# Kernel tuning notes

Measured on AMD Instinct MI355X. Metric: run time of the kernel, lower is better.

Reference implementation:

```python
import jax, jax.numpy as jnp
import numpy as np

B, T, M, C, H = 256, 512, 16, 16, 768  # batch, time, n_media, ctrl_dim, gru hidden


def setup_inputs() -> dict:
    key = jax.random.key(0)
    ks = jax.random.split(key, 16)
    def nrm(k, shape, s=0.05):
        return jax.random.normal(k, shape, jnp.float32) * s
    A = jnp.triu(jnp.ones((M, M), jnp.float32), 1)  # strict-upper DAG prior
    return dict(
        Xm=jax.random.uniform(ks[0], (B, T, M), jnp.float32),
        Xc=jax.random.normal(ks[1], (B, T, C), jnp.float32),
        R=jax.random.randint(ks[2], (B,), 0, 2),
        A=A,
        edge_w1=nrm(ks[3], (M, 2 * M)), edge_b1=jnp.zeros((M,), jnp.float32),
        edge_w2=nrm(ks[4], (M, M)), edge_b2=jnp.zeros((M,), jnp.float32),
        node_w=nrm(ks[5], (M, 2 * M)), node_b=jnp.zeros((M,), jnp.float32),
        W_ih=nrm(ks[6], (3 * H, M + C)), W_hh=nrm(ks[7], (3 * H, H)),
        b_ih=jnp.zeros((3 * H,), jnp.float32), b_hh=jnp.zeros((3 * H,), jnp.float32),
        wraw_w=nrm(ks[8], (M, H), 0.01), wraw_b=jnp.zeros((M,), jnp.float32),
        alpha=jnp.full((M,), 0.5, jnp.float32),
        hill_a=jax.random.uniform(ks[9], (M,), jnp.float32) * 0.8 + 0.6,
        hill_g=jax.random.uniform(ks[10], (M,), jnp.float32) * 0.3 + 0.1,
        ctrl_w=nrm(ks[11], (H, C)), ctrl_b=jnp.zeros((H,), jnp.float32),
        reg_emb=nrm(ks[12], (2, H)),
        bias=jnp.zeros((1,), jnp.float32),
        h0=jnp.zeros((1, 1, H), jnp.float32),
    )


def reference(Xm, Xc, R, A, edge_w1, edge_b1, edge_w2, edge_b2, node_w, node_b,
              W_ih, W_hh, b_ih, b_hh, wraw_w, wraw_b, alpha, hill_a, hill_g,
              ctrl_w, ctrl_b, reg_emb, bias, h0):
    Bq = Xm.shape[0]
    # --- CausalEncoder, fully batched over (B, T) ---
    send = Xm @ A.T                      # [B,T,M]
    recv = Xm @ A
    He = jax.nn.relu(jnp.concatenate([send, recv], -1) @ edge_w1.T + edge_b1)
    He = jax.nn.relu(He @ edge_w2.T + edge_b2)
    Z = jax.nn.relu(jnp.concatenate([Xm, He], -1) @ node_w.T + node_b)  # [B,T,M]
    # --- adstock: linear recurrence along time via scan ---
    a = jnp.clip(alpha, 0.0, 1.0)
    xt = jnp.swapaxes(Xm, 0, 1)          # [T,B,M]
    def ad_step(prev, x):
        cur = x + a * prev
        return cur, cur
    _, rest = jax.lax.scan(ad_step, xt[0], xt[1:])
    ads = jnp.swapaxes(jnp.concatenate([xt[:1], rest], 0), 0, 1)  # [B,T,M]
    cmax = jnp.maximum(jnp.max(ads, axis=1, keepdims=True), 1e-6)
    x_n = ads / cmax
    # --- hill saturation ---
    ha = jnp.clip(hill_a, 0.1, 3.0)
    hg = jnp.clip(hill_g, 0.1, 2.0)
    num = jnp.maximum(x_n, 0.0) ** ha
    hill = num / (num + hg ** ha + 1e-8)
    # --- GRU (PyTorch gate order r,z,n) via scan ---
    gru_in = jnp.concatenate([hill + Z, Xc], -1)       # [B,T,M+C]
    git = jnp.swapaxes(gru_in, 0, 1)                   # [T,B,M+C]
    h_init = jnp.broadcast_to(h0[0, 0], (Bq, h0.shape[-1]))
    def gru_step(h, x):
        gi = x @ W_ih.T + b_ih
        gh = h @ W_hh.T + b_hh
        ir, iz, inn = jnp.split(gi, 3, axis=-1)
        hr, hz, hn = jnp.split(gh, 3, axis=-1)
        r = jax.nn.sigmoid(ir + hr)
        z = jax.nn.sigmoid(iz + hz)
        n = jnp.tanh(inn + r * hn)
        h_new = (1.0 - z) * n + z * h
        return h_new, h_new
    _, hs = jax.lax.scan(gru_step, h_init, git)
    h_seq = jnp.swapaxes(hs, 0, 1)                     # [B,T,H]
    # --- coefficients + output heads ---
    w_pos = jax.nn.softplus(h_seq @ wraw_w.T + wraw_b)  # [B,T,M]
    w0 = 0.5 * jax.lax.stop_gradient(w_pos[:, 1]) + 0.5 * w_pos[:, 0]
    w_pos = w_pos.at[:, 0].set(w0)
    contrib = hill * w_pos
    media_term = contrib.sum(-1)                        # [B,T]
    ctrl_term = jax.nn.relu(Xc @ ctrl_w.T + ctrl_b).sum(-1) * 0.3
    reg_term = reg_emb[0].sum() * 0.3                   # original indexes with zeros
    y_scaled = media_term + ctrl_term + reg_term + bias[0]
    return y_scaled, w_pos, contrib
```

## Files before the change

### kernel.cpp

```cpp
#include <hip/hip_runtime.h>

typedef __bf16 bf16;
typedef bf16 bf16x8 __attribute__((ext_vector_type(8)));
typedef bf16 bf16x4 __attribute__((ext_vector_type(4)));
typedef float f32x4 __attribute__((ext_vector_type(4)));

#define MFMA16(a,b,c) __builtin_amdgcn_mfma_f32_16x16x32_bf16((a),(b),(c),0,0,0)

#define B_N 256
#define T_N 512
#define H_N 768
#define WROW 776
#define WIHROW 40

__device__ float    g_ctrl[B_N * T_N];
__device__ bf16     g_hbuf[2 * B_N * H_N];
__device__ unsigned g_flag[256 * 32];
__device__ unsigned g_members[8 * 32];
__device__ unsigned g_roster[8];
__device__ unsigned g_sync;

__device__ __forceinline__ float sigmoidf_(float x){ return 1.f/(1.f+__expf(-x)); }
__device__ __forceinline__ float tanhf_(float x){
  float e = __expf(-2.f*fabsf(x));
  float t = (1.f-e)/(1.f+e);
  return copysignf(t, x);
}
__device__ __forceinline__ float softplusf_(float x){
  return x > 20.f ? x : log1pf(__expf(x));
}

__global__ void k_zero() {
  const int tid = threadIdx.x;
  for (int i = tid; i < 256*32; i += 256) g_flag[i] = 0u;
  if (tid < 256) g_members[tid & 255] = 0u;
  if (tid < 8)   g_roster[tid] = 0u;
  if (tid == 0)  g_sync = 0u;
}

__global__ __launch_bounds__(256) void k_encode(
    const float* __restrict__ Xm, const float* __restrict__ Xc,
    const float* __restrict__ Aw,
    const float* __restrict__ ew1, const float* __restrict__ eb1,
    const float* __restrict__ ew2, const float* __restrict__ eb2,
    const float* __restrict__ nw,  const float* __restrict__ nb,
    const float* __restrict__ cw,  const float* __restrict__ cb,
    float* __restrict__ Zout)
{
  __shared__ float sA[16][16], sE1[16][32], sE2[16][16], sNW[16][32];
  __shared__ float sEB1[16], sEB2[16], sNB[16];
  __shared__ float sCW[768][16];
  __shared__ float sCB[768];
  const int tid = threadIdx.x;
  for (int i = tid; i < 256; i += 256) sA[i>>4][i&15] = Aw[i];
  for (int i = tid; i < 512; i += 256) sE1[i>>5][i&31] = ew1[i];
  for (int i = tid; i < 256; i += 256) sE2[i>>4][i&15] = ew2[i];
  for (int i = tid; i < 512; i += 256) sNW[i>>5][i&31] = nw[i];
  if (tid < 16) { sEB1[tid]=eb1[tid]; sEB2[tid]=eb2[tid]; sNB[tid]=nb[tid]; }
  for (int i = tid; i < 768*16; i += 256) sCW[i>>4][i&15] = cw[i];
  for (int i = tid; i < 768; i += 256) sCB[i] = cb[i];
  __syncthreads();
  const int idx = blockIdx.x*256 + tid;
  const float* xmp = Xm + (size_t)idx*16;
  const float* xcp = Xc + (size_t)idx*16;
  float xm[16], xc[16];
  #pragma unroll
  for (int j=0;j<4;j++){
    *(f32x4*)&xm[j*4] = *(const f32x4*)(xmp + j*4);
    *(f32x4*)&xc[j*4] = *(const f32x4*)(xcp + j*4);
  }
  float snd[16], rcv[16];
  #pragma unroll
  for (int i=0;i<16;i++){
    float s=0.f, r=0.f;
    #pragma unroll
    for (int j=0;j<16;j++){ s += xm[j]*sA[i][j]; r += xm[j]*sA[j][i]; }
    snd[i]=s; rcv[i]=r;
  }
  float he[16];
  #pragma unroll
  for (int i=0;i<16;i++){
    float a = sEB1[i];
    #pragma unroll
    for (int k=0;k<16;k++) a += snd[k]*sE1[i][k];
    #pragma unroll
    for (int k=0;k<16;k++) a += rcv[k]*sE1[i][16+k];
    he[i] = fmaxf(a, 0.f);
  }
  float he2[16];
  #pragma unroll
  for (int i=0;i<16;i++){
    float a = sEB2[i];
    #pragma unroll
    for (int k=0;k<16;k++) a += he[k]*sE2[i][k];
    he2[i] = fmaxf(a, 0.f);
  }
  float* zp = Zout + (size_t)idx*16;
  #pragma unroll
  for (int m=0;m<16;m++){
    float a = sNB[m];
    #pragma unroll
    for (int k=0;k<16;k++) a += xm[k]*sNW[m][k];
    #pragma unroll
    for (int k=0;k<16;k++) a += he2[k]*sNW[m][16+k];
    zp[m] = fmaxf(a, 0.f);
  }
  float cs = 0.f;
  for (int i=0;i<768;i++){
    float a = sCB[i];
    #pragma unroll
    for (int k=0;k<16;k++) a += xc[k]*sCW[i][k];
    cs += fmaxf(a, 0.f);
  }
  g_ctrl[idx] = cs * 0.3f;
}

__global__ __launch_bounds__(64) void k_adstock(
    const float* __restrict__ Xm, const float* __restrict__ alpha,
    const float* __restrict__ hill_a, const float* __restrict__ hill_g,
    float* __restrict__ Zio, float* __restrict__ hill_out)
{
  const int gid = blockIdx.x*64 + threadIdx.x;
  const int b = gid >> 4, m = gid & 15;
  float a  = fminf(fmaxf(alpha[m],  0.f),  1.f);
  float ha = fminf(fmaxf(hill_a[m], 0.1f), 3.f);
  float hg = fminf(fmaxf(hill_g[m], 0.1f), 2.f);
  float gpow = __powf(hg, ha);
  const float* xp = Xm + (size_t)b*T_N*16 + m;
  float prev = 0.f, cmax = 0.f;
  for (int t=0;t<T_N;t++){ float x = xp[(size_t)t*16]; prev = x + a*prev; cmax = fmaxf(cmax, prev); }
  cmax = fmaxf(cmax, 1e-6f);
  float inv = 1.f/cmax;
  prev = 0.f;
  float* zp  = Zio      + (size_t)b*T_N*16 + m;
  float* hp  = hill_out + (size_t)b*T_N*16 + m;
  for (int t=0;t<T_N;t++){
    float x = xp[(size_t)t*16];
    prev = x + a*prev;
    float xn  = fmaxf(prev*inv, 0.f);
    float num = __powf(xn, ha);
    float h   = num / (num + gpow + 1e-8f);
    float z   = zp[(size_t)t*16];
    hp[(size_t)t*16] = h;
    zp[(size_t)t*16] = h + z;
  }
}

__device__ __forceinline__ void poll_flags(unsigned midx, unsigned val) {
  int tries = 0;
  for (;;) {
    unsigned v = __hip_atomic_load(&g_flag[midx], __ATOMIC_RELAXED, __HIP_MEMORY_SCOPE_AGENT);
    if (__ballot(v >= val) == ~0ull) break;
    if (++tries > (1<<18)) break;
    if (tries > 8) __builtin_amdgcn_s_sleep(1);
  }
  __builtin_amdgcn_fence(__ATOMIC_ACQUIRE, "workgroup");
}

__global__ __launch_bounds__(256, 1) void k_gru(
    const float* __restrict__ Xc,
    const float* __restrict__ Wih, const float* __restrict__ Whh,
    const float* __restrict__ bih, const float* __restrict__ bhh,
    const float* __restrict__ wraww, const float* __restrict__ wrawb,
    const float* __restrict__ regemb, const float* __restrict__ bias,
    const float* __restrict__ h0,
    float* __restrict__ hillZ,
    float* __restrict__ hill,
    float* __restrict__ outy)
{
  __shared__ __align__(16) bf16 sW[88*WROW];
  __shared__ __align__(16) bf16 sWih[72*WIHROW];
  __shared__ float sGH[32][84];
  __shared__ float sGIN[32][36];
  __shared__ float sHm[32][24];
  __shared__ float sHD[32][17];
  __shared__ float sBih[72], sBhh[72];
  __shared__ float sWrb[16];
  __shared__ float sScal[2];
  __shared__ unsigned sGP[2];

  const int tid = threadIdx.x;
  const int wave = tid >> 6, lane = tid & 63;
  const int quad = lane >> 4, l16 = lane & 15;

  if (tid == 0) {
    unsigned x;
    asm volatile("s_getreg_b32 %0, hwreg(HW_REG_XCC_ID, 0, 32)" : "=s"(x));
    x &= 7u;
    unsigned slot = __hip_atomic_fetch_add(&g_roster[x], 1u,
                        __ATOMIC_RELAXED, __HIP_MEMORY_SCOPE_AGENT);
    if (slot < 32u)
      __hip_atomic_store(&g_members[x*32u + slot], (unsigned)blockIdx.x,
                         __ATOMIC_RELAXED, __HIP_MEMORY_SCOPE_AGENT);
    sGP[0] = x; sGP[1] = slot & 31u;
    __hip_atomic_fetch_add(&g_sync, 1u, __ATOMIC_RELEASE, __HIP_MEMORY_SCOPE_AGENT);
    int tries = 0;
    while (__hip_atomic_load(&g_sync, __ATOMIC_ACQUIRE, __HIP_MEMORY_SCOPE_AGENT) < 256u) {
      if (++tries > (1<<20)) break;
      __builtin_amdgcn_s_sleep(1);
    }
  }
  __syncthreads();
  const int g = (int)sGP[0], p = (int)sGP[1];
  const int j0 = p*24;
  const unsigned midx = __hip_atomic_load(&g_members[g*32 + (lane & 31)],
                            __ATOMIC_RELAXED, __HIP_MEMORY_SCOPE_AGENT) * 32u;
  const unsigned myflag = (unsigned)blockIdx.x * 32u;

  for (int c = tid; c < 88*192; c += 256) {
    int rl = c / 192, off = (c - rl*192)*4;
    const float* src = (rl < 72)
        ? &Whh[(size_t)((rl/24)*768 + j0 + (rl%24))*768 + off]
        : &wraww[(size_t)(rl-72)*768 + off];
    f32x4 w = *(const f32x4*)src;
    bf16x4 v; v[0]=(bf16)w[0]; v[1]=(bf16)w[1]; v[2]=(bf16)w[2]; v[3]=(bf16)w[3];
    *(bf16x4*)&sW[rl*WROW + off] = v;
  }
  for (int c = tid; c < 72*8; c += 256) {
    int rl = c >> 3, off = (c & 7)*4;
    int grow = (rl/24)*768 + j0 + (rl%24);
    f32x4 w = *(const f32x4*)&Wih[(size_t)grow*32 + off];
    bf16x4 v; v[0]=(bf16)w[0]; v[1]=(bf16)w[1]; v[2]=(bf16)w[2]; v[3]=(bf16)w[3];
    *(bf16x4*)&sWih[rl*WIHROW + off] = v;
  }
  if (tid < 72) {
    int grow = (tid/24)*768 + j0 + (tid%24);
    sBih[tid] = bih[grow];
    sBhh[tid] = bhh[grow];
  }
  if (tid >= 128 && tid < 144) sWrb[tid-128] = wrawb[tid-128];
  if (wave == 0) {
    float s = 0.f;
    for (int k = lane; k < 768; k += 64) s += regemb[k];
    #pragma unroll
    for (int off = 32; off; off >>= 1) s += __shfl_xor(s, off, 64);
    if (lane == 0) { sScal[0] = 0.3f*s; sScal[1] = bias[0]; }
  }
  {
    unsigned* hb = (unsigned*)g_hbuf;
    for (int e = tid; e < 384; e += 256) {
      int b = e/12, j = (e - b*12)*2;
      float f0 = h0[j0+j], f1 = h0[j0+j+1];
      sHm[b][j] = f0; sHm[b][j+1] = f1;
      union { bf16 h[2]; unsigned u; } pk;
      pk.h[0] = (bf16)f0; pk.h[1] = (bf16)f1;
      hb[((size_t)(g*32+b)*H_N + j0 + j) >> 1] = pk.u;
    }
  }
  __syncthreads();
  if (tid == 0)
    __hip_atomic_store(&g_flag[myflag], 1u, __ATOMIC_RELAXED, __HIP_MEMORY_SCOPE_AGENT);

  const int mi = wave >> 1;
  const bool lowN = !(wave & 1);
  const int batch_l = l16 + mi*16;
  const int gb = g*32 + batch_l;
  const int bq = g*32 + p;
  const float regt = sScal[0], bias0 = sScal[1];
  const int r0 = lowN ? l16        : 48 + l16;
  const int r1 = lowN ? 16 + l16   : min(64 + l16, 71);
  const int rX = lowN ? 32 + l16   : 72 + l16;
  const int rh = 72 + l16;

  bf16x8 bw0[24], bw1[24];
  #pragma unroll
  for (int kt = 0; kt < 24; kt++) {
    const int ko = kt*32 + quad*8;
    bw0[kt] = *(const bf16x8*)&sW[r0*WROW + ko];
    bw1[kt] = *(const bf16x8*)&sW[r1*WROW + ko];
  }
  const bf16x8 wf0 = *(const bf16x8*)&sWih[r0*WIHROW + quad*8];
  const bf16x8 wf1 = *(const bf16x8*)&sWih[r1*WIHROW + quad*8];
  const bf16x8 wf2 = lowN ? *(const bf16x8*)&sWih[(32+l16)*WIHROW + quad*8] : wf0;

  float wp0_r = 0.f, hl0_r = 0.f, ct0_r = 0.f;

  f32x4 xf0, xf1;
  {
    const float* hz = hillZ + (size_t)gb*T_N*16;
    const float* xr = Xc    + (size_t)gb*T_N*16;
    const float* src = (quad < 2) ? (hz + quad*8) : (xr + (quad-2)*8);
    xf0 = *(const f32x4*)src;
    xf1 = *(const f32x4*)(src + 4);
  }
  float hl_pf = 0.f, ct_pf = 0.f;
  if (tid < 16) {
    hl_pf = hill[(size_t)bq*T_N*16 + tid];
    if (tid == 0) ct_pf = g_ctrl[(size_t)bq*T_N];
  }

  const bf16* hb_base = g_hbuf;
  int par = 0;
  for (int t = 0; t < T_N; t++) {
    f32x4 a0 = {0.f,0.f,0.f,0.f}, a1 = a0, a2 = a0, gi0 = a0, gi1 = a0, hd = a0;
    {
      bf16x8 ax;
      ax[0]=(bf16)xf0[0]; ax[1]=(bf16)xf0[1]; ax[2]=(bf16)xf0[2]; ax[3]=(bf16)xf0[3];
      ax[4]=(bf16)xf1[0]; ax[5]=(bf16)xf1[1]; ax[6]=(bf16)xf1[2]; ax[7]=(bf16)xf1[3];
      if (lowN) {
        a0 = MFMA16(ax, wf0, a0);
        a1 = MFMA16(ax, wf1, a1);
        a2 = MFMA16(ax, wf2, a2);
      } else {
        gi0 = MFMA16(ax, wf0, gi0);
        gi1 = MFMA16(ax, wf1, gi1);
      }
    }
    poll_flags(midx, (unsigned)(t + 1));
    bf16x8 hf[24];
    {
      const bf16* hrow = hb_base + (size_t)par*B_N*H_N + (size_t)gb*H_N + quad*8;
      #pragma unroll
      for (int kt = 0; kt < 24; kt++) {
        asm volatile("global_load_dwordx4 %0, %1, off sc0"
                     : "=v"(hf[kt]) : "v"(hrow + kt*32) : "memory");
      }
      asm volatile("s_waitcnt vmcnt(0)"
          : "+v"(hf[0]),"+v"(hf[1]),"+v"(hf[2]),"+v"(hf[3]),
            "+v"(hf[4]),"+v"(hf[5]),"+v"(hf[6]),"+v"(hf[7]) :: "memory");
      asm volatile(""
          : "+v"(hf[8]),"+v"(hf[9]),"+v"(hf[10]),"+v"(hf[11]),
            "+v"(hf[12]),"+v"(hf[13]),"+v"(hf[14]),"+v"(hf[15]));
      asm volatile(""
          : "+v"(hf[16]),"+v"(hf[17]),"+v"(hf[18]),"+v"(hf[19]),
            "+v"(hf[20]),"+v"(hf[21]),"+v"(hf[22]),"+v"(hf[23]));
    }
    {
      const int tn = (t + 1 < T_N) ? t + 1 : T_N - 1;
      const float* hz = hillZ + ((size_t)gb*T_N + tn)*16;
      const float* xr = Xc    + ((size_t)gb*T_N + tn)*16;
      const float* src = (quad < 2) ? (hz + quad*8) : (xr + (quad-2)*8);
      xf0 = *(const f32x4*)src;
      xf1 = *(const f32x4*)(src + 4);
    }
    #pragma unroll
    for (int kt = 0; kt < 24; kt++) {
      const int ko = kt*32 + quad*8;
      a0 = MFMA16(hf[kt], bw0[kt], a0);
      a1 = MFMA16(hf[kt], bw1[kt], a1);
      if (lowN) a2 = MFMA16(hf[kt], *(const bf16x8*)&sW[rX*WROW + ko], a2);
      else      hd = MFMA16(hf[kt], *(const bf16x8*)&sW[rX*WROW + ko], hd);
    }
    {
      const int rb = mi*16 + quad*4;
      const int c0 = lowN ? l16 : 48 + l16;
      const int c1 = lowN ? 16 + l16 : 64 + l16;
      #pragma unroll
      for (int r = 0; r < 4; r++) {
        sGH[rb + r][c0] = a0[r];
        sGH[rb + r][c1] = a1[r];
        if (lowN) sGH[rb + r][32 + l16] = a2[r];
        else { sGIN[rb + r][l16] = gi0[r]; sGIN[rb + r][16 + l16] = gi1[r];
               sHD[rb + r][l16] = hd[r]; }
      }
    }
    __syncthreads();
    float hd_s = 0.f;
    if (tid < 16) hd_s = sHD[p][tid];
    if (tid >= 32) {
      unsigned* hnxt = (unsigned*)(g_hbuf + (size_t)(1-par)*B_N*H_N);
      for (int e = tid - 32; e < 384; e += 224) {
        int b = e/12, j = (e - b*12)*2;
        float hn0, hn1;
        {
          float rr = sigmoidf_(sGH[b][j]    + sBih[j]    + sBhh[j]);
          float zz = sigmoidf_(sGH[b][24+j] + sBih[24+j] + sBhh[24+j]);
          float hh = sGH[b][48+j] + sBhh[48+j];
          float in_ = sGIN[b][j]  + sBih[48+j];
          float nn = tanhf_(in_ + rr*hh);
          hn0 = (1.f-zz)*nn + zz*sHm[b][j];
        }
        {
          int j1 = j+1;
          float rr = sigmoidf_(sGH[b][j1]    + sBih[j1]    + sBhh[j1]);
          float zz = sigmoidf_(sGH[b][24+j1] + sBih[24+j1] + sBhh[24+j1]);
          float hh = sGH[b][48+j1] + sBhh[48+j1];
          float in_ = sGIN[b][j1]  + sBih[48+j1];
          float nn = tanhf_(in_ + rr*hh);
          hn1 = (1.f-zz)*nn + zz*sHm[b][j1];
        }
        sHm[b][j] = hn0; sHm[b][j+1] = hn1;
        union { bf16 h[2]; unsigned u; } pk;
        pk.h[0] = (bf16)hn0; pk.h[1] = (bf16)hn1;
        hnxt[((size_t)(g*32+b)*H_N + j0 + j) >> 1] = pk.u;
      }
    }
    __syncthreads();
    if (tid == 0)
      __hip_atomic_store(&g_flag[myflag], (unsigned)(t + 2), __ATOMIC_RELAXED, __HIP_MEMORY_SCOPE_AGENT);
    if (t > 0 && tid < 16) {
      const int tt = t - 1;
      float wp = softplusf_(hd_s + sWrb[tid]);
      float hl = hl_pf;
      if (tt == 0) { wp0_r = wp; hl0_r = hl; ct0_r = ct_pf; }
      else {
        size_t o = (size_t)bq*T_N + tt;
        float cv = hl*wp;
        hillZ[o*16 + tid] = wp;
        hill[o*16 + tid]  = cv;
        float cs = cv;
        cs += __shfl_xor(cs, 8, 64);
        cs += __shfl_xor(cs, 4, 64);
        cs += __shfl_xor(cs, 2, 64);
        cs += __shfl_xor(cs, 1, 64);
        if (tid == 0) outy[o] = cs + ct_pf + regt + bias0;
        if (tt == 1) {
          float w0 = 0.5f*(wp + wp0_r);
          float c0v = hl0_r*w0;
          size_t o0 = (size_t)bq*T_N;
          hillZ[o0*16 + tid] = w0;
          hill[o0*16 + tid]  = c0v;
          float cs0 = c0v;
          cs0 += __shfl_xor(cs0, 8, 64);
          cs0 += __shfl_xor(cs0, 4, 64);
          cs0 += __shfl_xor(cs0, 2, 64);
          cs0 += __shfl_xor(cs0, 1, 64);
          if (tid == 0) outy[o0] = cs0 + ct0_r + regt + bias0;
        }
      }
    }
    if (tid < 16) {
      hl_pf = hill[((size_t)bq*T_N + t)*16 + tid];
      if (tid == 0) ct_pf = g_ctrl[(size_t)bq*T_N + t];
    }
    par ^= 1;
  }
  if (wave & 1) {
    poll_flags(midx, (unsigned)(T_N + 1));
    const bf16* hrow = hb_base + (size_t)par*B_N*H_N + (size_t)gb*H_N + quad*8;
    f32x4 hd = {0.f,0.f,0.f,0.f};
    bf16x8 hf[24];
    #pragma unroll
    for (int kt = 0; kt < 24; kt++) {
      asm volatile("global_load_dwordx4 %0, %1, off sc0"
                   : "=v"(hf[kt]) : "v"(hrow + kt*32) : "memory");
    }
    asm volatile("s_waitcnt vmcnt(0)"
        : "+v"(hf[0]),"+v"(hf[1]),"+v"(hf[2]),"+v"(hf[3]),
          "+v"(hf[4]),"+v"(hf[5]),"+v"(hf[6]),"+v"(hf[7]) :: "memory");
    asm volatile(""
        : "+v"(hf[8]),"+v"(hf[9]),"+v"(hf[10]),"+v"(hf[11]),
          "+v"(hf[12]),"+v"(hf[13]),"+v"(hf[14]),"+v"(hf[15]));
    asm volatile(""
        : "+v"(hf[16]),"+v"(hf[17]),"+v"(hf[18]),"+v"(hf[19]),
          "+v"(hf[20]),"+v"(hf[21]),"+v"(hf[22]),"+v"(hf[23]));
    #pragma unroll
    for (int kt = 0; kt < 24; kt++) {
      const int ko = kt*32 + quad*8;
      hd = MFMA16(hf[kt], *(const bf16x8*)&sW[rh*WROW + ko], hd);
    }
    const int rb = mi*16 + quad*4;
    #pragma unroll
    for (int r = 0; r < 4; r++) sHD[rb + r][l16] = hd[r];
  }
  __syncthreads();
  if (tid < 16) {
    const int tt = T_N - 1;
    float wp = softplusf_(sHD[p][tid] + sWrb[tid]);
    float hl = hill[((size_t)bq*T_N + tt)*16 + tid];
    size_t o = (size_t)bq*T_N + tt;
    float cv = hl*wp;
    hillZ[o*16 + tid] = wp;
    hill[o*16 + tid]  = cv;
    float cs = cv;
    cs += __shfl_xor(cs, 8, 64);
    cs += __shfl_xor(cs, 4, 64);
    cs += __shfl_xor(cs, 2, 64);
    cs += __shfl_xor(cs, 1, 64);
    if (tid == 0) outy[o] = cs + g_ctrl[o] + regt + bias0;
  }
}

extern "C" void kernel_launch(void* const* d_in, const int* in_sizes, int n_in,
                              void* d_out, int out_size, void* d_ws, size_t ws_size,
                              hipStream_t stream) {
  const float* Xm    = (const float*)d_in[0];
  const float* Xc    = (const float*)d_in[1];
  const float* Aw    = (const float*)d_in[3];
  const float* ew1   = (const float*)d_in[4];
  const float* eb1   = (const float*)d_in[5];
  const float* ew2   = (const float*)d_in[6];
  const float* eb2   = (const float*)d_in[7];
  const float* nw    = (const float*)d_in[8];
  const float* nb    = (const float*)d_in[9];
  const float* Wih   = (const float*)d_in[10];
  const float* Whh   = (const float*)d_in[11];
  const float* bih   = (const float*)d_in[12];
  const float* bhh   = (const float*)d_in[13];
  const float* wraww = (const float*)d_in[14];
  const float* wrawb = (const float*)d_in[15];
  const float* alpha = (const float*)d_in[16];
  const float* hilla = (const float*)d_in[17];
  const float* hillg = (const float*)d_in[18];
  const float* cw    = (const float*)d_in[19];
  const float* cb    = (const float*)d_in[20];
  const float* regemb= (const float*)d_in[21];
  const float* bias  = (const float*)d_in[22];
  const float* h0    = (const float*)d_in[23];

  float* outy = (float*)d_out;
  float* outw = outy + 256*512;
  float* outc = outw + 256*512*16;

  k_zero<<<1, 256, 0, stream>>>();
  k_encode<<<512, 256, 0, stream>>>(Xm, Xc, Aw, ew1, eb1, ew2, eb2, nw, nb, cw, cb,
                                    outw);
  k_adstock<<<64, 64, 0, stream>>>(Xm, alpha, hilla, hillg, outw, outc);
  k_gru<<<dim3(256), dim3(256), 0, stream>>>(
      Xc, Wih, Whh, bih, bhh, wraww, wrawb, regemb, bias, h0,
      outw, outc, outy);
}
```

Before: 3.584 ms.

## Split GRU batch into two half-groups and pipeline MFMA with gate update wave

Restructures the persistent GRU kernel so each block handles its 32 batch rows as two 16-row halves. Three waves run the recurrent MFMAs for one half while a fourth wave applies the gate nonlinearities and publishes h for the other half, with separate per-half flags. Weight fragments move into registers loaded straight from global memory, and the h loads are split into staged waitcnts that interleave with even/odd accumulators. This aims to hide cross-block sync and gate-math latency behind matrix work. The cost is a more intricate flag protocol with timeout-based polling and extra barriers per half-step.

```diff
diff --git a/kernel.cpp b/kernel.cpp
--- a/kernel.cpp
+++ b/kernel.cpp
@@ -4,6 +4,7 @@
 typedef bf16 bf16x8 __attribute__((ext_vector_type(8)));
 typedef bf16 bf16x4 __attribute__((ext_vector_type(4)));
 typedef float f32x4 __attribute__((ext_vector_type(4)));
+typedef float f32x2 __attribute__((ext_vector_type(2)));
 
 #define MFMA16(a,b,c) __builtin_amdgcn_mfma_f32_16x16x32_bf16((a),(b),(c),0,0,0)
 
@@ -11,11 +12,10 @@
 #define T_N 512
 #define H_N 768
 #define WROW 776
-#define WIHROW 40
 
 __device__ float    g_ctrl[B_N * T_N];
 __device__ bf16     g_hbuf[2 * B_N * H_N];
-__device__ unsigned g_flag[256 * 32];
+__device__ unsigned g_flag[256 * 64];
 __device__ unsigned g_members[8 * 32];
 __device__ unsigned g_roster[8];
 __device__ unsigned g_sync;
@@ -29,11 +29,19 @@
 __device__ __forceinline__ float softplusf_(float x){
   return x > 20.f ? x : log1pf(__expf(x));
 }
+__device__ __forceinline__ bf16x8 ld_bf8(const float* p){
+  f32x4 a = *(const f32x4*)p;
+  f32x4 b = *(const f32x4*)(p + 4);
+  bf16x8 v;
+  v[0]=(bf16)a[0]; v[1]=(bf16)a[1]; v[2]=(bf16)a[2]; v[3]=(bf16)a[3];
+  v[4]=(bf16)b[0]; v[5]=(bf16)b[1]; v[6]=(bf16)b[2]; v[7]=(bf16)b[3];
+  return v;
+}
 
 __global__ void k_zero() {
   const int tid = threadIdx.x;
-  for (int i = tid; i < 256*32; i += 256) g_flag[i] = 0u;
-  if (tid < 256) g_members[tid & 255] = 0u;
+  for (int i = tid; i < 256*64; i += 256) g_flag[i] = 0u;
+  if (tid < 256) g_members[tid] = 0u;
   if (tid < 8)   g_roster[tid] = 0u;
   if (tid == 0)  g_sync = 0u;
 }
@@ -146,16 +154,20 @@
   }
 }
 
-__device__ __forceinline__ void poll_flags(unsigned midx, unsigned val) {
-  int tries = 0;
+__device__ __forceinline__ bool poll_flags(unsigned midx, unsigned val) {
+  int tries = 0; bool ok = true;
   for (;;) {
     unsigned v = __hip_atomic_load(&g_flag[midx], __ATOMIC_RELAXED, __HIP_MEMORY_SCOPE_AGENT);
     if (__ballot(v >= val) == ~0ull) break;
-    if (++tries > (1<<18)) break;
+    if (++tries > (1<<18)) { ok = false; break; }
     if (tries > 8) __builtin_amdgcn_s_sleep(1);
   }
   __builtin_amdgcn_fence(__ATOMIC_ACQUIRE, "workgroup");
-}
+  return ok;
+}
+
+#define HL(i, OFF) asm volatile("global_load_dwordx4 %0, %1, off offset:" OFF " sc0" \
+      : "=v"(hf[i]) : "v"(hsrc) : "memory")
 
 __global__ __launch_bounds__(256, 1) void k_gru(
     const float* __restrict__ Xc,
@@ -168,16 +180,15 @@
     float* __restrict__ hill,
     float* __restrict__ outy)
 {
-  __shared__ __align__(16) bf16 sW[88*WROW];
-  __shared__ __align__(16) bf16 sWih[72*WIHROW];
-  __shared__ float sGH[32][84];
-  __shared__ float sGIN[32][36];
-  __shared__ float sHm[32][24];
-  __shared__ float sHD[32][17];
-  __shared__ float sBih[72], sBhh[72];
+  __shared__ __align__(16) bf16 sW2[48*WROW];
+  __shared__ __align__(16) float sGH2[2][16][100];
+  __shared__ __align__(16) float sGIN[2][16][32];
+  __shared__ __align__(16) float sHm[32][28];
+  __shared__ __align__(16) float sBih[72], sBhh[72];
   __shared__ float sWrb[16];
   __shared__ float sScal[2];
   __shared__ unsigned sGP[2];
+  __shared__ unsigned sTok[2];
 
   const int tid = threadIdx.x;
   const int wave = tid >> 6, lane = tid & 63;
@@ -193,6 +204,7 @@
       __hip_atomic_store(&g_members[x*32u + slot], (unsigned)blockIdx.x,
                          __ATOMIC_RELAXED, __HIP_MEMORY_SCOPE_AGENT);
     sGP[0] = x; sGP[1] = slot & 31u;
+    sTok[0] = 0u; sTok[1] = 0u;
     __hip_atomic_fetch_add(&g_sync, 1u, __ATOMIC_RELEASE, __HIP_MEMORY_SCOPE_AGENT);
     int tries = 0;
     while (__hip_atomic_load(&g_sync, __ATOMIC_ACQUIRE, __HIP_MEMORY_SCOPE_AGENT) < 256u) {
@@ -203,25 +215,23 @@
   __syncthreads();
   const int g = (int)sGP[0], p = (int)sGP[1];
   const int j0 = p*24;
-  const unsigned midx = __hip_atomic_load(&g_members[g*32 + (lane & 31)],
-                            __ATOMIC_RELAXED, __HIP_MEMORY_SCOPE_AGENT) * 32u;
-  const unsigned myflag = (unsigned)blockIdx.x * 32u;
-
-  for (int c = tid; c < 88*192; c += 256) {
+  const int s_own = (p >= 16) ? 1 : 0;
+  const int bqL = p & 15;
+  const int bq = g*32 + p;
+  const unsigned member = __hip_atomic_load(&g_members[g*32 + (lane & 31)],
+                              __ATOMIC_RELAXED, __HIP_MEMORY_SCOPE_AGENT);
+  const unsigned midx0 = member * 64u;
+  const unsigned myflag = (unsigned)blockIdx.x * 64u;
+
+  for (int c = tid; c < 48*192; c += 256) {
     int rl = c / 192, off = (c - rl*192)*4;
-    const float* src = (rl < 72)
-        ? &Whh[(size_t)((rl/24)*768 + j0 + (rl%24))*768 + off]
-        : &wraww[(size_t)(rl-72)*768 + off];
-    f32x4 w = *(const f32x4*)src;
+    int L = (rl < 16) ? (16 + rl) : ((rl < 32) ? (32 + rl) : (48 + rl));
+    f32x4 w;
+    if (L < 72)      w = *(const f32x4*)&Whh[(size_t)((L/24)*768 + j0 + (L%24))*768 + off];
+    else if (L < 88) w = *(const f32x4*)&wraww[(size_t)(L-72)*768 + off];
+    else             { w[0]=0.f; w[1]=0.f; w[2]=0.f; w[3]=0.f; }
     bf16x4 v; v[0]=(bf16)w[0]; v[1]=(bf16)w[1]; v[2]=(bf16)w[2]; v[3]=(bf16)w[3];
-    *(bf16x4*)&sW[rl*WROW + off] = v;
-  }
-  for (int c = tid; c < 72*8; c += 256) {
-    int rl = c >> 3, off = (c & 7)*4;
-    int grow = (rl/24)*768 + j0 + (rl%24);
-    f32x4 w = *(const f32x4*)&Wih[(size_t)grow*32 + off];
-    bf16x4 v; v[0]=(bf16)w[0]; v[1]=(bf16)w[1]; v[2]=(bf16)w[2]; v[3]=(bf16)w[3];
-    *(bf16x4*)&sWih[rl*WIHROW + off] = v;
+    *(bf16x4*)&sW2[rl*WROW + off] = v;
   }
   if (tid < 72) {
     int grow = (tid/24)*768 + j0 + (tid%24);
@@ -230,12 +240,39 @@
   }
   if (tid >= 128 && tid < 144) sWrb[tid-128] = wrawb[tid-128];
   if (wave == 0) {
-    float s = 0.f;
-    for (int k = lane; k < 768; k += 64) s += regemb[k];
-    #pragma unroll
-    for (int off = 32; off; off >>= 1) s += __shfl_xor(s, off, 64);
-    if (lane == 0) { sScal[0] = 0.3f*s; sScal[1] = bias[0]; }
-  }
+    float sacc = 0.f;
+    for (int k = lane; k < 768; k += 64) sacc += regemb[k];
+    #pragma unroll
+    for (int off = 32; off; off >>= 1) sacc += __shfl_xor(sacc, off, 64);
+    if (lane == 0) { sScal[0] = 0.3f*sacc; sScal[1] = bias[0]; }
+  }
+
+  bf16x8 bw[24];
+  bf16x8 wf0, wf1, wfg;
+  #pragma unroll
+  for (int i = 0; i < 8; i++) { wf0[i]=(bf16)0.f; wf1[i]=(bf16)0.f; wfg[i]=(bf16)0.f; }
+  if (wave < 3) {
+    const int L = wave*32 + l16;
+    const float* rowA = (L < 72)
+        ? Whh + (size_t)((L/24)*768 + j0 + (L%24))*768
+        : wraww + (size_t)(L-72)*768;
+    #pragma unroll
+    for (int kk = 0; kk < 24; kk++) bw[kk] = ld_bf8(rowA + kk*32 + quad*8);
+    if (wave == 0) {
+      const int La = l16, Lb = 16 + l16;
+      wf0 = ld_bf8(Wih + (size_t)((La/24)*768 + j0 + (La%24))*32 + quad*8);
+      wf1 = ld_bf8(Wih + (size_t)((Lb/24)*768 + j0 + (Lb%24))*32 + quad*8);
+    } else if (wave == 1) {
+      const int La = 32 + l16, Lb = 48 + l16;
+      wf0 = ld_bf8(Wih + (size_t)((La/24)*768 + j0 + (La%24))*32 + quad*8);
+      wfg = ld_bf8(Wih + (size_t)((Lb/24)*768 + j0 + (Lb%24))*32 + quad*8);
+    } else {
+      const int Lb = 64 + l16;
+      if (Lb < 72)
+        wfg = ld_bf8(Wih + (size_t)((Lb/24)*768 + j0 + (Lb%24))*32 + quad*8);
+    }
+  }
+
   {
     unsigned* hb = (unsigned*)g_hbuf;
     for (int e = tid; e < 384; e += 256) {
@@ -248,215 +285,244 @@
     }
   }
   __syncthreads();
-  if (tid == 0)
-    __hip_atomic_store(&g_flag[myflag], 1u, __ATOMIC_RELAXED, __HIP_MEMORY_SCOPE_AGENT);
-
-  const int mi = wave >> 1;
-  const bool lowN = !(wave & 1);
-  const int batch_l = l16 + mi*16;
-  const int gb = g*32 + batch_l;
-  const int bq = g*32 + p;
+  if (tid == 0) {
+    __hip_atomic_store(&g_flag[myflag],      1u, __ATOMIC_RELAXED, __HIP_MEMORY_SCOPE_AGENT);
+    __hip_atomic_store(&g_flag[myflag + 32], 1u, __ATOMIC_RELAXED, __HIP_MEMORY_SCOPE_AGENT);
+  }
   const float regt = sScal[0], bias0 = sScal[1];
-  const int r0 = lowN ? l16        : 48 + l16;
-  const int r1 = lowN ? 16 + l16   : min(64 + l16, 71);
-  const int rX = lowN ? 32 + l16   : 72 + l16;
-  const int rh = 72 + l16;
-
-  bf16x8 bw0[24], bw1[24];
-  #pragma unroll
-  for (int kt = 0; kt < 24; kt++) {
-    const int ko = kt*32 + quad*8;
-    bw0[kt] = *(const bf16x8*)&sW[r0*WROW + ko];
-    bw1[kt] = *(const bf16x8*)&sW[r1*WROW + ko];
-  }
-  const bf16x8 wf0 = *(const bf16x8*)&sWih[r0*WIHROW + quad*8];
-  const bf16x8 wf1 = *(const bf16x8*)&sWih[r1*WIHROW + quad*8];
-  const bf16x8 wf2 = lowN ? *(const bf16x8*)&sWih[(32+l16)*WIHROW + quad*8] : wf0;
 
   float wp0_r = 0.f, hl0_r = 0.f, ct0_r = 0.f;
+  float hl_pf = 0.f, ct_pf = 0.f;
+  if (wave == 3 && lane < 16) {
+    hl_pf = hill[(size_t)bq*T_N*16 + lane];
+    if (lane == 0) ct_pf = g_ctrl[(size_t)bq*T_N];
+  }
 
   f32x4 xf0, xf1;
-  {
-    const float* hz = hillZ + (size_t)gb*T_N*16;
-    const float* xr = Xc    + (size_t)gb*T_N*16;
-    const float* src = (quad < 2) ? (hz + quad*8) : (xr + (quad-2)*8);
-    xf0 = *(const f32x4*)src;
-    xf1 = *(const f32x4*)(src + 4);
-  }
-  float hl_pf = 0.f, ct_pf = 0.f;
-  if (tid < 16) {
-    hl_pf = hill[(size_t)bq*T_N*16 + tid];
-    if (tid == 0) ct_pf = g_ctrl[(size_t)bq*T_N];
-  }
-
-  const bf16* hb_base = g_hbuf;
-  int par = 0;
-  for (int t = 0; t < T_N; t++) {
-    f32x4 a0 = {0.f,0.f,0.f,0.f}, a1 = a0, a2 = a0, gi0 = a0, gi1 = a0, hd = a0;
-    {
-      bf16x8 ax;
-      ax[0]=(bf16)xf0[0]; ax[1]=(bf16)xf0[1]; ax[2]=(bf16)xf0[2]; ax[3]=(bf16)xf0[3];
-      ax[4]=(bf16)xf1[0]; ax[5]=(bf16)xf1[1]; ax[6]=(bf16)xf1[2]; ax[7]=(bf16)xf1[3];
-      if (lowN) {
-        a0 = MFMA16(ax, wf0, a0);
-        a1 = MFMA16(ax, wf1, a1);
-        a2 = MFMA16(ax, wf2, a2);
-      } else {
-        gi0 = MFMA16(ax, wf0, gi0);
-        gi1 = MFMA16(ax, wf1, gi1);
-      }
-    }
-    poll_flags(midx, (unsigned)(t + 1));
-    bf16x8 hf[24];
-    {
-      const bf16* hrow = hb_base + (size_t)par*B_N*H_N + (size_t)gb*H_N + quad*8;
-      #pragma unroll
-      for (int kt = 0; kt < 24; kt++) {
-        asm volatile("global_load_dwordx4 %0, %1, off sc0"
-                     : "=v"(hf[kt]) : "v"(hrow + kt*32) : "memory");
-      }
-      asm volatile("s_waitcnt vmcnt(0)"
+  xf0[0]=0.f; xf0[1]=0.f; xf0[2]=0.f; xf0[3]=0.f; xf1 = xf0;
+  if (wave < 3) {
+    const int gb0 = g*32 + l16;
+    const float* srcx = (quad < 2)
+        ? hillZ + (size_t)gb0*T_N*16 + quad*8
+        : Xc    + (size_t)gb0*T_N*16 + (quad-2)*8;
+    xf0 = *(const f32x4*)srcx;
+    xf1 = *(const f32x4*)(srcx + 4);
+  }
+  const bf16* wlds = &sW2[(size_t)(wave*16 + l16)*WROW + quad*8];
+
+  #pragma unroll 1
+  for (int k = 0; k <= 2*T_N; k++) {
+    const int t = k >> 1, s = k & 1;
+    if (wave < 3) {
+      if (k < 2*T_N) {
+        {
+          unsigned tok = sTok[s];
+          if (tok < (unsigned)(t + 1))
+            poll_flags(midx0 + (unsigned)(s*32), (unsigned)(t + 1));
+          else
+            __builtin_amdgcn_fence(__ATOMIC_ACQUIRE, "workgroup");
+        }
+        const bf16* hsrc = g_hbuf + (size_t)(t&1)*B_N*H_N
+                         + (size_t)(g*32 + s*16 + l16)*H_N + quad*8;
+        f32x4 xn0, xn1;
+        {
+          const int sn = s ^ 1;
+          int tn = s ? (t + 1) : t; if (tn >= T_N) tn = T_N - 1;
+          const int gbn = g*32 + sn*16 + l16;
+          const float* srcx = (quad < 2)
+              ? hillZ + ((size_t)gbn*T_N + tn)*16 + quad*8
+              : Xc    + ((size_t)gbn*T_N + tn)*16 + (quad-2)*8;
+          asm volatile("global_load_dwordx4 %0, %2, off\n\t"
+                       "global_load_dwordx4 %1, %2, off offset:16"
+                       : "=v"(xn0), "=v"(xn1) : "v"(srcx) : "memory");
+        }
+        bf16x8 hf[24];
+        HL(0,"0");    HL(1,"64");   HL(2,"128");  HL(3,"192");
+        HL(4,"256");  HL(5,"320");  HL(6,"384");  HL(7,"448");
+        HL(8,"512");  HL(9,"576");  HL(10,"640"); HL(11,"704");
+        HL(12,"768"); HL(13,"832"); HL(14,"896"); HL(15,"960");
+        HL(16,"1024");HL(17,"1088");HL(18,"1152");HL(19,"1216");
+        HL(20,"1280");HL(21,"1344");HL(22,"1408");HL(23,"1472");
+        bf16x8 ax;
+        ax[0]=(bf16)xf0[0]; ax[1]=(bf16)xf0[1]; ax[2]=(bf16)xf0[2]; ax[3]=(bf16)xf0[3];
+        ax[4]=(bf16)xf1[0]; ax[5]=(bf16)xf1[1]; ax[6]=(bf16)xf1[2]; ax[7]=(bf16)xf1[3];
+        f32x4 az; az[0]=0.f; az[1]=0.f; az[2]=0.f; az[3]=0.f;
+        f32x4 a0e=az, a0o=az, a1e=az, a1o=az, gi=az;
+        if (wave == 0)      { a0e = MFMA16(ax, wf0, a0e); a1e = MFMA16(ax, wf1, a1e); }
+        else if (wave == 1) { a0e = MFMA16(ax, wf0, a0e); gi  = MFMA16(ax, wfg, gi);  }
+        else                { gi  = MFMA16(ax, wfg, gi); }
+        asm volatile("s_waitcnt vmcnt(16)"
           : "+v"(hf[0]),"+v"(hf[1]),"+v"(hf[2]),"+v"(hf[3]),
             "+v"(hf[4]),"+v"(hf[5]),"+v"(hf[6]),"+v"(hf[7]) :: "memory");
-      asm volatile(""
+        #pragma unroll
+        for (int kk = 0; kk < 8; kk += 2) {
+          a0e = MFMA16(hf[kk],   bw[kk],   a0e);
+          a1e = MFMA16(hf[kk],   *(const bf16x8*)&wlds[kk*32],     a1e);
+          a0o = MFMA16(hf[kk+1], bw[kk+1], a0o);
+          a1o = MFMA16(hf[kk+1], *(const bf16x8*)&wlds[(kk+1)*32], a1o);
+        }
+        asm volatile("s_waitcnt vmcnt(8)"
           : "+v"(hf[8]),"+v"(hf[9]),"+v"(hf[10]),"+v"(hf[11]),
-            "+v"(hf[12]),"+v"(hf[13]),"+v"(hf[14]),"+v"(hf[15]));
-      asm volatile(""
+            "+v"(hf[12]),"+v"(hf[13]),"+v"(hf[14]),"+v"(hf[15]) :: "memory");
+        #pragma unroll
+        for (int kk = 8; kk < 16; kk += 2) {
+          a0e = MFMA16(hf[kk],   bw[kk],   a0e);
+          a1e = MFMA16(hf[kk],   *(const bf16x8*)&wlds[kk*32],     a1e);
+          a0o = MFMA16(hf[kk+1], bw[kk+1], a0o);
+          a1o = MFMA16(hf[kk+1], *(const bf16x8*)&wlds[(kk+1)*32], a1o);
+        }
+        asm volatile("s_waitcnt vmcnt(0)"
           : "+v"(hf[16]),"+v"(hf[17]),"+v"(hf[18]),"+v"(hf[19]),
-            "+v"(hf[20]),"+v"(hf[21]),"+v"(hf[22]),"+v"(hf[23]));
-    }
-    {
-      const int tn = (t + 1 < T_N) ? t + 1 : T_N - 1;
-      const float* hz = hillZ + ((size_t)gb*T_N + tn)*16;
-      const float* xr = Xc    + ((size_t)gb*T_N + tn)*16;
-      const float* src = (quad < 2) ? (hz + quad*8) : (xr + (quad-2)*8);
-      xf0 = *(const f32x4*)src;
-      xf1 = *(const f32x4*)(src + 4);
-    }
-    #pragma unroll
-    for (int kt = 0; kt < 24; kt++) {
-      const int ko = kt*32 + quad*8;
-      a0 = MFMA16(hf[kt], bw0[kt], a0);
-      a1 = MFMA16(hf[kt], bw1[kt], a1);
-      if (lowN) a2 = MFMA16(hf[kt], *(const bf16x8*)&sW[rX*WROW + ko], a2);
-      else      hd = MFMA16(hf[kt], *(const bf16x8*)&sW[rX*WROW + ko], hd);
-    }
-    {
-      const int rb = mi*16 + quad*4;
-      const int c0 = lowN ? l16 : 48 + l16;
-      const int c1 = lowN ? 16 + l16 : 64 + l16;
+            "+v"(hf[20]),"+v"(hf[21]),"+v"(hf[22]),"+v"(hf[23]),
+            "+v"(xn0),"+v"(xn1) :: "memory");
+        #pragma unroll
+        for (int kk = 16; kk < 24; kk += 2) {
+          a0e = MFMA16(hf[kk],   bw[kk],   a0e);
+          a1e = MFMA16(hf[kk],   *(const bf16x8*)&wlds[kk*32],     a1e);
+          a0o = MFMA16(hf[kk+1], bw[kk+1], a0o);
+          a1o = MFMA16(hf[kk+1], *(const bf16x8*)&wlds[(kk+1)*32], a1o);
+        }
+        xf0 = xn0; xf1 = xn1;
+        f32x4 A0 = a0e + a0o, A1 = a1e + a1o;
+        {
+          const int c0 = wave*32 + l16;
+          #pragma unroll
+          for (int r = 0; r < 4; r++) {
+            const int rb = quad*4 + r;
+            sGH2[s][rb][c0]    = A0[r];
+            sGH2[s][rb][c0+16] = A1[r];
+          }
+          if (wave == 1) {
+            #pragma unroll
+            for (int r = 0; r < 4; r++) sGIN[s][quad*4 + r][l16] = gi[r];
+          } else if (wave == 2) {
+            #pragma unroll
+            for (int r = 0; r < 4; r++) sGIN[s][quad*4 + r][16 + l16] = gi[r];
+          }
+        }
+      }
+    } else if (k > 0) {
+      const int pt = (k-1) >> 1, ps = (k-1) & 1;
+      const int b = lane >> 2, jp = (lane & 3) * 6;
+      const int bg = ps*16 + b;
+      float hn[6];
       #pragma unroll
-      for (int r = 0; r < 4; r++) {
-        sGH[rb + r][c0] = a0[r];
-        sGH[rb + r][c1] = a1[r];
-        if (lowN) sGH[rb + r][32 + l16] = a2[r];
-        else { sGIN[rb + r][l16] = gi0[r]; sGIN[rb + r][16 + l16] = gi1[r];
-               sHD[rb + r][l16] = hd[r]; }
+      for (int u = 0; u < 6; u += 2) {
+        f32x2 gr  = *(const f32x2*)&sGH2[ps][b][jp+u];
+        f32x2 gz  = *(const f32x2*)&sGH2[ps][b][24+jp+u];
+        f32x2 gn  = *(const f32x2*)&sGH2[ps][b][48+jp+u];
+        f32x2 gi2 = *(const f32x2*)&sGIN[ps][b][jp+u];
+        f32x2 hm  = *(const f32x2*)&sHm[bg][jp+u];
+        f32x2 bir = *(const f32x2*)&sBih[jp+u],    bhr = *(const f32x2*)&sBhh[jp+u];
+        f32x2 biz = *(const f32x2*)&sBih[24+jp+u], bhz = *(const f32x2*)&sBhh[24+jp+u];
+        f32x2 bin_= *(const f32x2*)&sBih[48+jp+u], bhn = *(const f32x2*)&sBhh[48+jp+u];
+        #pragma unroll
+        for (int v = 0; v < 2; v++) {
+          float rr = sigmoidf_(gr[v] + bir[v] + bhr[v]);
+          float zz = sigmoidf_(gz[v] + biz[v] + bhz[v]);
+          float nn = tanhf_(gi2[v] + bin_[v] + rr*(gn[v] + bhn[v]));
+          hn[u+v] = (1.f - zz)*nn + zz*hm[v];
+        }
+        f32x2 st; st[0] = hn[u]; st[1] = hn[u+1];
+        *(f32x2*)&sHm[bg][jp+u] = st;
+      }
+      {
+        unsigned* hb = (unsigned*)(g_hbuf + (size_t)((pt+1)&1)*B_N*H_N);
+        const size_t eb = ((size_t)(g*32+bg)*H_N + j0 + jp) >> 1;
+        #pragma unroll
+        for (int u = 0; u < 3; u++) {
+          union { bf16 h[2]; unsigned w; } pk;
+          pk.h[0] = (bf16)hn[2*u]; pk.h[1] = (bf16)hn[2*u+1];
+          hb[eb + u] = pk.w;
+        }
+      }
+      asm volatile("s_waitcnt vmcnt(0)" ::: "memory");
+      if (lane == 0)
+        __hip_atomic_store(&g_flag[myflag + ps*32], (unsigned)(pt + 2),
+                           __ATOMIC_RELAXED, __HIP_MEMORY_SCOPE_AGENT);
+      if (poll_flags(midx0 + (unsigned)(ps*32), (unsigned)(pt + 2))) {
+        if (lane == 0) sTok[ps] = (unsigned)(pt + 2);
+      }
+      if (ps == s_own && lane < 16) {
+        if (pt > 0) {
+          const int tt = pt - 1;
+          float wp = softplusf_(sGH2[ps][bqL][72+lane] + sWrb[lane]);
+          float hl = hl_pf;
+          if (tt == 0) { wp0_r = wp; hl0_r = hl; ct0_r = ct_pf; }
+          else {
+            size_t o = (size_t)bq*T_N + tt;
+            float cv = hl*wp;
+            hillZ[o*16 + lane] = wp;
+            hill[o*16 + lane]  = cv;
+            float cs = cv;
+            cs += __shfl_xor(cs, 8, 64);
+            cs += __shfl_xor(cs, 4, 64);
+            cs += __shfl_xor(cs, 2, 64);
+            cs += __shfl_xor(cs, 1, 64);
+            if (lane == 0) outy[o] = cs + ct_pf + regt + bias0;
+            if (tt == 1) {
+              float w0 = 0.5f*(wp + wp0_r);
+              float c0v = hl0_r*w0;
+              size_t o0 = (size_t)bq*T_N;
+              hillZ[o0*16 + lane] = w0;
+              hill[o0*16 + lane]  = c0v;
+              float cs0 = c0v;
+              cs0 += __shfl_xor(cs0, 8, 64);
+              cs0 += __shfl_xor(cs0, 4, 64);
+              cs0 += __shfl_xor(cs0, 2, 64);
+              cs0 += __shfl_xor(cs0, 1, 64);
+              if (lane == 0) outy[o0] = cs0 + ct0_r + regt + bias0;
+            }
+          }
+        }
+        hl_pf = hill[((size_t)bq*T_N + pt)*16 + lane];
+        if (lane == 0) ct_pf = g_ctrl[(size_t)bq*T_N + pt];
       }
     }
     __syncthreads();
-    float hd_s = 0.f;
-    if (tid < 16) hd_s = sHD[p][tid];
-    if (tid >= 32) {
-      unsigned* hnxt = (unsigned*)(g_hbuf + (size_t)(1-par)*B_N*H_N);
-      for (int e = tid - 32; e < 384; e += 224) {
-        int b = e/12, j = (e - b*12)*2;
-        float hn0, hn1;
-        {
-          float rr = sigmoidf_(sGH[b][j]    + sBih[j]    + sBhh[j]);
-          float zz = sigmoidf_(sGH[b][24+j] + sBih[24+j] + sBhh[24+j]);
-          float hh = sGH[b][48+j] + sBhh[48+j];
-          float in_ = sGIN[b][j]  + sBih[48+j];
-          float nn = tanhf_(in_ + rr*hh);
-          hn0 = (1.f-zz)*nn + zz*sHm[b][j];
-        }
-        {
-          int j1 = j+1;
-          float rr = sigmoidf_(sGH[b][j1]    + sBih[j1]    + sBhh[j1]);
-          float zz = sigmoidf_(sGH[b][24+j1] + sBih[24+j1] + sBhh[24+j1]);
-          float hh = sGH[b][48+j1] + sBhh[48+j1];
-          float in_ = sGIN[b][j1]  + sBih[48+j1];
-          float nn = tanhf_(in_ + rr*hh);
-          hn1 = (1.f-zz)*nn + zz*sHm[b][j1];
-        }
-        sHm[b][j] = hn0; sHm[b][j+1] = hn1;
-        union { bf16 h[2]; unsigned u; } pk;
-        pk.h[0] = (bf16)hn0; pk.h[1] = (bf16)hn1;
-        hnxt[((size_t)(g*32+b)*H_N + j0 + j) >> 1] = pk.u;
-      }
+  }
+
+  if (wave == 2) {
+    poll_flags(midx0 + (unsigned)(s_own*32), (unsigned)(T_N + 1));
+    const bf16* hsrc = g_hbuf + (size_t)((T_N)&1)*B_N*H_N
+                     + (size_t)(g*32 + s_own*16 + l16)*H_N + quad*8;
+    bf16x8 hf[24];
+    HL(0,"0");    HL(1,"64");   HL(2,"128");  HL(3,"192");
+    HL(4,"256");  HL(5,"320");  HL(6,"384");  HL(7,"448");
+    HL(8,"512");  HL(9,"576");  HL(10,"640"); HL(11,"704");
+    HL(12,"768"); HL(13,"832"); HL(14,"896"); HL(15,"960");
+    HL(16,"1024");HL(17,"1088");HL(18,"1152");HL(19,"1216");
+    HL(20,"1280");HL(21,"1344");HL(22,"1408");HL(23,"1472");
+    asm volatile("s_waitcnt vmcnt(0)"
+      : "+v"(hf[0]),"+v"(hf[1]),"+v"(hf[2]),"+v"(hf[3]),
+        "+v"(hf[4]),"+v"(hf[5]),"+v"(hf[6]),"+v"(hf[7]) :: "memory");
+    asm volatile(""
+      : "+v"(hf[8]),"+v"(hf[9]),"+v"(hf[10]),"+v"(hf[11]),
+        "+v"(hf[12]),"+v"(hf[13]),"+v"(hf[14]),"+v"(hf[15]));
+    asm volatile(""
+      : "+v"(hf[16]),"+v"(hf[17]),"+v"(hf[18]),"+v"(hf[19]),
+        "+v"(hf[20]),"+v"(hf[21]),"+v"(hf[22]),"+v"(hf[23]));
+    f32x4 az; az[0]=0.f; az[1]=0.f; az[2]=0.f; az[3]=0.f;
+    f32x4 a0e=az, a0o=az, a1e=az, a1o=az;
+    #pragma unroll
+    for (int kk = 0; kk < 24; kk += 2) {
+      a0e = MFMA16(hf[kk],   bw[kk],   a0e);
+      a1e = MFMA16(hf[kk],   *(const bf16x8*)&wlds[kk*32],     a1e);
+      a0o = MFMA16(hf[kk+1], bw[kk+1], a0o);
+      a1o = MFMA16(hf[kk+1], *(const bf16x8*)&wlds[(kk+1)*32], a1o);
     }
-    __syncthreads();
-    if (tid == 0)
-      __hip_atomic_store(&g_flag[myflag], (unsigned)(t + 2), __ATOMIC_RELAXED, __HIP_MEMORY_SCOPE_AGENT);
-    if (t > 0 && tid < 16) {
-      const int tt = t - 1;
-      float wp = softplusf_(hd_s + sWrb[tid]);
-      float hl = hl_pf;
-      if (tt == 0) { wp0_r = wp; hl0_r = hl; ct0_r = ct_pf; }
-      else {
-        size_t o = (size_t)bq*T_N + tt;
-        float cv = hl*wp;
-        hillZ[o*16 + tid] = wp;
-        hill[o*16 + tid]  = cv;
-        float cs = cv;
-        cs += __shfl_xor(cs, 8, 64);
-        cs += __shfl_xor(cs, 4, 64);
-        cs += __shfl_xor(cs, 2, 64);
-        cs += __shfl_xor(cs, 1, 64);
-        if (tid == 0) outy[o] = cs + ct_pf + regt + bias0;
-        if (tt == 1) {
-          float w0 = 0.5f*(wp + wp0_r);
-          float c0v = hl0_r*w0;
-          size_t o0 = (size_t)bq*T_N;
-          hillZ[o0*16 + tid] = w0;
-          hill[o0*16 + tid]  = c0v;
-          float cs0 = c0v;
-          cs0 += __shfl_xor(cs0, 8, 64);
-          cs0 += __shfl_xor(cs0, 4, 64);
-          cs0 += __shfl_xor(cs0, 2, 64);
-          cs0 += __shfl_xor(cs0, 1, 64);
-          if (tid == 0) outy[o0] = cs0 + ct0_r + regt + bias0;
-        }
-      }
+    f32x4 A0 = a0e + a0o, A1 = a1e + a1o;
+    #pragma unroll
+    for (int r = 0; r < 4; r++) {
+      const int rb = quad*4 + r;
+      sGH2[0][rb][64 + l16] = A0[r];
+      sGH2[0][rb][80 + l16] = A1[r];
     }
-    if (tid < 16) {
-      hl_pf = hill[((size_t)bq*T_N + t)*16 + tid];
-      if (tid == 0) ct_pf = g_ctrl[(size_t)bq*T_N + t];
-    }
-    par ^= 1;
-  }
-  if (wave & 1) {
-    poll_flags(midx, (unsigned)(T_N + 1));
-    const bf16* hrow = hb_base + (size_t)par*B_N*H_N + (size_t)gb*H_N + quad*8;
-    f32x4 hd = {0.f,0.f,0.f,0.f};
-    bf16x8 hf[24];
-    #pragma unroll
-    for (int kt = 0; kt < 24; kt++) {
-      asm volatile("global_load_dwordx4 %0, %1, off sc0"
-                   : "=v"(hf[kt]) : "v"(hrow + kt*32) : "memory");
-    }
-    asm volatile("s_waitcnt vmcnt(0)"
-        : "+v"(hf[0]),"+v"(hf[1]),"+v"(hf[2]),"+v"(hf[3]),
-          "+v"(hf[4]),"+v"(hf[5]),"+v"(hf[6]),"+v"(hf[7]) :: "memory");
-    asm volatile(""
-        : "+v"(hf[8]),"+v"(hf[9]),"+v"(hf[10]),"+v"(hf[11]),
-          "+v"(hf[12]),"+v"(hf[13]),"+v"(hf[14]),"+v"(hf[15]));
-    asm volatile(""
-        : "+v"(hf[16]),"+v"(hf[17]),"+v"(hf[18]),"+v"(hf[19]),
-          "+v"(hf[20]),"+v"(hf[21]),"+v"(hf[22]),"+v"(hf[23]));
-    #pragma unroll
-    for (int kt = 0; kt < 24; kt++) {
-      const int ko = kt*32 + quad*8;
-      hd = MFMA16(hf[kt], *(const bf16x8*)&sW[rh*WROW + ko], hd);
-    }
-    const int rb = mi*16 + quad*4;
-    #pragma unroll
-    for (int r = 0; r < 4; r++) sHD[rb + r][l16] = hd[r];
   }
   __syncthreads();
   if (tid < 16) {
     const int tt = T_N - 1;
-    float wp = softplusf_(sHD[p][tid] + sWrb[tid]);
+    float wp = softplusf_(sGH2[0][bqL][72+tid] + sWrb[tid]);
     float hl = hill[((size_t)bq*T_N + tt)*16 + tid];
     size_t o = (size_t)bq*T_N + tt;
     float cv = hl*wp;
```

Result: slower. 4.287 ms (+19.6%).
